# Kernel tuning notes

Measured on AMD Instinct MI355X. Metric: run time of the kernel, lower is better.

The kernel has to match this reference:

```python
import jax, jax.numpy as jnp
import numpy as np

NQ, NH = 7, 4          # quantiles x horizons
G = NQ * NH            # 28 independent branches
IN_DIM, H1, H2 = 64, 64, 32


def setup_inputs() -> dict:
    key = jax.random.key(0)
    ks = jax.random.split(key, 7)
    B = 131072
    x = jax.random.normal(ks[0], (B, IN_DIM), dtype=jnp.float32)
    s1 = 1.0 / np.sqrt(IN_DIM)
    s2 = 1.0 / np.sqrt(H1)
    s3 = 1.0 / np.sqrt(H2)
    W1 = jax.random.uniform(ks[1], (G, IN_DIM, H1), jnp.float32, -s1, s1)
    b1 = jax.random.uniform(ks[2], (G, H1), jnp.float32, -s1, s1)
    W2 = jax.random.uniform(ks[3], (G, H1, H2), jnp.float32, -s2, s2)
    b2 = jax.random.uniform(ks[4], (G, H2), jnp.float32, -s2, s2)
    W3 = jax.random.uniform(ks[5], (G, H2, 1), jnp.float32, -s3, s3)
    b3 = jax.random.uniform(ks[6], (G, 1), jnp.float32, -s3, s3)
    return {"x": x, "W1": W1, "b1": b1, "W2": W2, "b2": b2, "W3": W3, "b3": b3}


def reference(x, W1, b1, W2, b2, W3, b3):
    # All G branches fused as batched GEMMs. x: [B, in]
    B = x.shape[0]
    h = jax.nn.relu(jnp.einsum('bi,gij->gbj', x, W1) + b1[:, None, :])   # [G,B,H1]
    h = jax.nn.relu(jnp.einsum('gbj,gjk->gbk', h, W2) + b2[:, None, :])  # [G,B,H2]
    o = jnp.einsum('gbk,gko->gbo', h, W3) + b3[:, None, :]               # [G,B,1]
    # branch order matches nested loop: quantile outer, horizon inner
    out = o[..., 0].reshape(NQ, NH, B).transpose(2, 0, 1)                # [B,NQ,NH]
    return out
```

## Files before the change

kernel.cpp:

```cpp
#include <hip/hip_runtime.h>
#include <hip/hip_bf16.h>
#include <hip/hip_fp16.h>

#define GN 28
#define G_TILE_BYTES 12288
#define WS_BYTES (GN * G_TILE_BYTES)

typedef __attribute__((ext_vector_type(4))) float f32x4;
typedef __attribute__((ext_vector_type(8))) short short8;
typedef _Float16 f16x8 __attribute__((ext_vector_type(8)));
typedef __fp16 pk16x2 __attribute__((ext_vector_type(2)));

__device__ __forceinline__ unsigned short f2h(float v){
  __half h = __float2half(v);
  return __builtin_bit_cast(unsigned short, h);
}
__device__ __forceinline__ f32x4 mfma16f(short8 a, short8 b, f32x4 c){
  return __builtin_amdgcn_mfma_f32_16x16x32_f16(
      __builtin_bit_cast(f16x8, a), __builtin_bit_cast(f16x8, b), c, 0, 0, 0);
}

__global__ __launch_bounds__(256) void prep_weights(
    const float* __restrict__ W1, const float* __restrict__ W2,
    unsigned char* __restrict__ ws){
  __shared__ float t1[64*65];
  __shared__ float t2[64*33];
  const int g = blockIdx.x;
  const int tid = threadIdx.x;

  {
    const f32x4* src = (const f32x4*)(W1 + g*4096);
    int k = tid >> 2, n0 = (tid & 3) * 16;
    #pragma unroll
    for (int j = 0; j < 4; ++j){
      f32x4 v = src[tid*4 + j];
      #pragma unroll
      for (int e = 0; e < 4; ++e) t1[k*65 + n0 + j*4 + e] = v[e];
    }
  }
  {
    const f32x4* src = (const f32x4*)(W2 + g*2048);
    int k = tid >> 2, n0 = (tid & 3) * 8;
    #pragma unroll
    for (int j = 0; j < 2; ++j){
      f32x4 v = src[tid*2 + j];
      #pragma unroll
      for (int e = 0; e < 4; ++e) t2[k*33 + n0 + j*4 + e] = v[e];
    }
  }
  __syncthreads();

  unsigned char* base = ws + g*G_TILE_BYTES;
  {
    int n = tid & 63, mh = tid >> 6;
    #pragma unroll
    for (int h = 0; h < 2; ++h){
      unsigned w[4];
      #pragma unroll
      for (int mm = 0; mm < 4; ++mm){
        int m = mh*8 + h*4 + mm;
        float lo = t1[(2*m    )*65 + n];
        float hi = t1[(2*m + 1)*65 + n];
        w[mm] = (unsigned)f2h(lo) | ((unsigned)f2h(hi) << 16);
      }
      int off = (n*128 + mh*32 + h*16) ^ ((n & 7) << 4);
      *(uint4*)(base + off) = make_uint4(w[0], w[1], w[2], w[3]);
    }
  }
  {
    int n2 = tid & 31, mq = tid >> 5;
    unsigned w[4];
    #pragma unroll
    for (int mm = 0; mm < 4; ++mm){
      int m = mq*4 + mm;
      int kk = 2*m;
      int ks = kk >> 5, qq = (kk >> 3) & 3, u = (kk >> 2) & 1, i = kk & 3;
      int kn = 32*ks + 16*u + 4*qq + i;
      float lo = t2[(kn    )*33 + n2];
      float hi = t2[(kn + 1)*33 + n2];
      w[mm] = (unsigned)f2h(lo) | ((unsigned)f2h(hi) << 16);
    }
    int off = (n2*128 + mq*16) ^ ((n2 & 7) << 4);
    *(uint4*)(base + 8192 + off) = make_uint4(w[0], w[1], w[2], w[3]);
  }
}

__global__ __launch_bounds__(256, 4) void mlp_fused(
    const float* __restrict__ x,  const float* __restrict__ b1,
    const float* __restrict__ b2, const float* __restrict__ W3,
    const float* __restrict__ b3, const unsigned char* __restrict__ ws,
    float* __restrict__ out){
  __shared__ uint4 wbuf[2][768];
  __shared__ float outb[128*28];

  const int tid = threadIdx.x;
  const int wv  = tid >> 6;
  const int ln  = tid & 63;
  const int l15 = ln & 15;
  const int q   = ln >> 4;
  const int rowBase = blockIdx.x * 128 + wv * 32;

  short8 xf[2][2];
  #pragma unroll
  for (int rt = 0; rt < 2; ++rt)
    #pragma unroll
    for (int ks = 0; ks < 2; ++ks){
      const float* p = x + (rowBase + rt*16 + l15)*64 + ks*32 + q*8;
      f32x4 a = *(const f32x4*)p;
      f32x4 b = *(const f32x4*)(p + 4);
      short8 s;
      #pragma unroll
      for (int j = 0; j < 4; ++j){
        s[j]   = (short)f2h(a[j]);
        s[4+j] = (short)f2h(b[j]);
      }
      xf[rt][ks] = s;
    }

  int offA1[4][2], offA2[2][2];
  #pragma unroll
  for (int nt = 0; nt < 4; ++nt)
    #pragma unroll
    for (int ks = 0; ks < 2; ++ks){
      int n = nt*16 + l15;
      offA1[nt][ks] = ((n*128 + ks*64 + q*16) ^ ((n & 7) << 4)) >> 4;
    }
  #pragma unroll
  for (int nt = 0; nt < 2; ++nt)
    #pragma unroll
    for (int ks = 0; ks < 2; ++ks){
      int n2 = nt*16 + l15;
      offA2[nt][ks] = (((n2*128 + ks*64 + q*16) ^ ((n2 & 7) << 4)) >> 4) + 512;
    }

  auto stage = [&](int g, int buf){
    const unsigned char* gb = ws + g*G_TILE_BYTES + wv*3072 + ln*16;
    uint4* lb = &wbuf[buf][wv*192];
    #pragma unroll
    for (int it = 0; it < 3; ++it){
      __builtin_amdgcn_global_load_lds(
          (const __attribute__((address_space(1))) void*)(gb + it*1024),
          (__attribute__((address_space(3))) void*)(lb + it*64), 16, 0, 0);
    }
  };

  auto packrelu = [&](const f32x4& v0, const f32x4& v1) -> short8 {
    union { unsigned u[4]; short8 s; } r;
    pk16x2 t0 = __builtin_amdgcn_cvt_pkrtz(fmaxf(v0[0],0.f), fmaxf(v0[1],0.f));
    pk16x2 t1 = __builtin_amdgcn_cvt_pkrtz(fmaxf(v0[2],0.f), fmaxf(v0[3],0.f));
    pk16x2 t2 = __builtin_amdgcn_cvt_pkrtz(fmaxf(v1[0],0.f), fmaxf(v1[1],0.f));
    pk16x2 t3 = __builtin_amdgcn_cvt_pkrtz(fmaxf(v1[2],0.f), fmaxf(v1[3],0.f));
    r.u[0] = __builtin_bit_cast(unsigned, t0);
    r.u[1] = __builtin_bit_cast(unsigned, t1);
    r.u[2] = __builtin_bit_cast(unsigned, t2);
    r.u[3] = __builtin_bit_cast(unsigned, t3);
    return r.s;
  };

  auto body = [&](int g, f32x4 (&bC)[4], f32x4 (&bN)[4]){
    const int cur = g & 1;
    if (g + 1 < GN) stage(g + 1, cur ^ 1);

    const int gnext = (g + 1 < GN) ? g + 1 : GN - 1;
    #pragma unroll
    for (int nt = 0; nt < 4; ++nt)
      bN[nt] = *(const f32x4*)(b1 + gnext*64 + nt*16 + q*4);

    const uint4* wb = wbuf[cur];

    short8 a1[4][2];
    #pragma unroll
    for (int nt = 0; nt < 4; ++nt)
      #pragma unroll
      for (int ks = 0; ks < 2; ++ks)
        a1[nt][ks] = __builtin_bit_cast(short8, wb[offA1[nt][ks]]);
    f32x4 acc1[4][2];
    #pragma unroll
    for (int nt = 0; nt < 4; ++nt)
      #pragma unroll
      for (int rt = 0; rt < 2; ++rt){
        acc1[nt][rt] = mfma16f(a1[nt][0], xf[rt][0], bC[nt]);
        acc1[nt][rt] = mfma16f(a1[nt][1], xf[rt][1], acc1[nt][rt]);
      }

    f32x4 b2v[2], w3v[2];
    #pragma unroll
    for (int nt = 0; nt < 2; ++nt){
      b2v[nt] = *(const f32x4*)(b2 + g*32 + nt*16 + q*4);
      w3v[nt] = *(const f32x4*)(W3 + g*32 + nt*16 + q*4);
    }

    short8 bh[2][2];
    #pragma unroll
    for (int rt = 0; rt < 2; ++rt)
      #pragma unroll
      for (int ks = 0; ks < 2; ++ks)
        bh[rt][ks] = packrelu(acc1[2*ks][rt], acc1[2*ks + 1][rt]);

    short8 a2[2][2];
    #pragma unroll
    for (int nt = 0; nt < 2; ++nt)
      #pragma unroll
      for (int ks = 0; ks < 2; ++ks)
        a2[nt][ks] = __builtin_bit_cast(short8, wb[offA2[nt][ks]]);
    f32x4 acc2[2][2];
    #pragma unroll
    for (int nt = 0; nt < 2; ++nt)
      #pragma unroll
      for (int rt = 0; rt < 2; ++rt){
        acc2[nt][rt] = mfma16f(a2[nt][0], bh[rt][0], b2v[nt]);
        acc2[nt][rt] = mfma16f(a2[nt][1], bh[rt][1], acc2[nt][rt]);
      }

    float bias3 = b3[g];
    #pragma unroll
    for (int rt = 0; rt < 2; ++rt){
      float p = 0.0f;
      #pragma unroll
      for (int nt = 0; nt < 2; ++nt)
        #pragma unroll
        for (int i = 0; i < 4; ++i)
          p = fmaf(fmaxf(acc2[nt][rt][i], 0.0f), w3v[nt][i], p);
      p += __shfl_xor(p, 16);
      p += __shfl_xor(p, 32);
      p += bias3;
      if (ln < 16)
        outb[(wv*32 + rt*16 + ln)*28 + g] = p;
    }

    asm volatile("s_waitcnt vmcnt(0)" ::: "memory");
    __syncthreads();
  };

  f32x4 b1A[4], b1B[4];
  stage(0, 0);
  #pragma unroll
  for (int nt = 0; nt < 4; ++nt)
    b1A[nt] = *(const f32x4*)(b1 + 0*64 + nt*16 + q*4);
  asm volatile("s_waitcnt vmcnt(0)" ::: "memory");
  __syncthreads();

  for (int gg = 0; gg < GN; gg += 2){
    body(gg,     b1A, b1B);
    body(gg + 1, b1B, b1A);
  }

  const uint2* ob2 = (const uint2*)outb;
  uint2* og2 = (uint2*)(out + blockIdx.x * (128*28));
  #pragma unroll
  for (int i = 0; i < 7; ++i){
    int idx = i*256 + tid;
    og2[idx] = ob2[idx];
  }
}

extern "C" void kernel_launch(void* const* d_in, const int* in_sizes, int n_in,
                              void* d_out, int out_size, void* d_ws, size_t ws_size,
                              hipStream_t stream){
  const float* x  = (const float*)d_in[0];
  const float* W1 = (const float*)d_in[1];
  const float* b1 = (const float*)d_in[2];
  const float* W2 = (const float*)d_in[3];
  const float* b2 = (const float*)d_in[4];
  const float* W3 = (const float*)d_in[5];
  const float* b3 = (const float*)d_in[6];
  unsigned char* ws = (unsigned char*)d_ws;
  float* out = (float*)d_out;
  if (ws_size < (size_t)WS_BYTES) return;
  hipLaunchKernelGGL(prep_weights, dim3(GN), dim3(256), 0, stream, W1, W2, ws);
  hipLaunchKernelGGL(mlp_fused, dim3(1024), dim3(256), 0, stream,
                     x, b1, b2, W3, b3, ws, out);
}
```

Measured before the change: 144.3 us.

## Stage weights in chunks of three branches to cut barriers per block

Restructures the branch loop so each double-buffered LDS stage holds three branches' weights, which cuts the number of vmcnt waits and block barriers from 28 to 10. The output staging buffer is shrunk to a per-chunk double buffer, and each chunk's three columns are written straight to global memory with scalar strided stores. LDS use grows to roughly 76KB per block, so launch bounds drop to 2 blocks per CU, which lowers occupancy. The new output writes are narrow and uncoalesced.

```diff
diff --git a/kernel.cpp b/kernel.cpp
--- a/kernel.cpp
+++ b/kernel.cpp
@@ -3,6 +3,8 @@
 #include <hip/hip_fp16.h>
 
 #define GN 28
+#define CH 3
+#define NCH 10
 #define G_TILE_BYTES 12288
 #define WS_BYTES (GN * G_TILE_BYTES)
 
@@ -85,13 +87,13 @@
   }
 }
 
-__global__ __launch_bounds__(256, 4) void mlp_fused(
+__global__ __launch_bounds__(256, 2) void mlp_fused(
     const float* __restrict__ x,  const float* __restrict__ b1,
     const float* __restrict__ b2, const float* __restrict__ W3,
     const float* __restrict__ b3, const unsigned char* __restrict__ ws,
     float* __restrict__ out){
-  __shared__ uint4 wbuf[2][768];
-  __shared__ float outb[128*28];
+  __shared__ uint4 wbuf[2][CH*768];
+  __shared__ float outb[2][128*CH];
 
   const int tid = threadIdx.x;
   const int wv  = tid >> 6;
@@ -133,14 +135,20 @@
       offA2[nt][ks] = (((n2*128 + ks*64 + q*16) ^ ((n2 & 7) << 4)) >> 4) + 512;
     }
 
-  auto stage = [&](int g, int buf){
-    const unsigned char* gb = ws + g*G_TILE_BYTES + wv*3072 + ln*16;
-    uint4* lb = &wbuf[buf][wv*192];
-    #pragma unroll
-    for (int it = 0; it < 3; ++it){
-      __builtin_amdgcn_global_load_lds(
-          (const __attribute__((address_space(1))) void*)(gb + it*1024),
-          (__attribute__((address_space(3))) void*)(lb + it*64), 16, 0, 0);
+  auto stageChunk = [&](int ch, int buf){
+    #pragma unroll
+    for (int t = 0; t < CH; ++t){
+      int g = ch*CH + t;
+      if (g < GN){
+        const unsigned char* gb = ws + g*G_TILE_BYTES + wv*3072 + ln*16;
+        uint4* lb = &wbuf[buf][t*768 + wv*192];
+        #pragma unroll
+        for (int it = 0; it < 3; ++it){
+          __builtin_amdgcn_global_load_lds(
+              (const __attribute__((address_space(1))) void*)(gb + it*1024),
+              (__attribute__((address_space(3))) void*)(lb + it*64), 16, 0, 0);
+        }
+      }
     }
   };
 
@@ -157,100 +165,102 @@
     return r.s;
   };
 
-  auto body = [&](int g, f32x4 (&bC)[4], f32x4 (&bN)[4]){
-    const int cur = g & 1;
-    if (g + 1 < GN) stage(g + 1, cur ^ 1);
-
-    const int gnext = (g + 1 < GN) ? g + 1 : GN - 1;
-    #pragma unroll
-    for (int nt = 0; nt < 4; ++nt)
-      bN[nt] = *(const f32x4*)(b1 + gnext*64 + nt*16 + q*4);
-
+  stageChunk(0, 0);
+  asm volatile("s_waitcnt vmcnt(0)" ::: "memory");
+  __syncthreads();
+
+  for (int ch = 0; ch < NCH; ++ch){
+    const int cur = ch & 1;
+    if (ch + 1 < NCH) stageChunk(ch + 1, cur ^ 1);
     const uint4* wb = wbuf[cur];
-
-    short8 a1[4][2];
-    #pragma unroll
-    for (int nt = 0; nt < 4; ++nt)
-      #pragma unroll
-      for (int ks = 0; ks < 2; ++ks)
-        a1[nt][ks] = __builtin_bit_cast(short8, wb[offA1[nt][ks]]);
-    f32x4 acc1[4][2];
-    #pragma unroll
-    for (int nt = 0; nt < 4; ++nt)
+    float* ob = &outb[cur][0];
+
+    #pragma unroll
+    for (int t = 0; t < CH; ++t){
+      const int g = ch*CH + t;
+      if (g >= GN) continue;
+      const uint4* wt = wb + t*768;
+
+      f32x4 b1v[4];
+      #pragma unroll
+      for (int nt = 0; nt < 4; ++nt)
+        b1v[nt] = *(const f32x4*)(b1 + g*64 + nt*16 + q*4);
+
+      short8 a1[4][2];
+      #pragma unroll
+      for (int nt = 0; nt < 4; ++nt)
+        #pragma unroll
+        for (int ks = 0; ks < 2; ++ks)
+          a1[nt][ks] = __builtin_bit_cast(short8, wt[offA1[nt][ks]]);
+      f32x4 acc1[4][2];
+      #pragma unroll
+      for (int nt = 0; nt < 4; ++nt)
+        #pragma unroll
+        for (int rt = 0; rt < 2; ++rt){
+          acc1[nt][rt] = mfma16f(a1[nt][0], xf[rt][0], b1v[nt]);
+          acc1[nt][rt] = mfma16f(a1[nt][1], xf[rt][1], acc1[nt][rt]);
+        }
+
+      f32x4 b2v[2], w3v[2];
+      #pragma unroll
+      for (int nt = 0; nt < 2; ++nt){
+        b2v[nt] = *(const f32x4*)(b2 + g*32 + nt*16 + q*4);
+        w3v[nt] = *(const f32x4*)(W3 + g*32 + nt*16 + q*4);
+      }
+
+      short8 bh[2][2];
+      #pragma unroll
+      for (int rt = 0; rt < 2; ++rt)
+        #pragma unroll
+        for (int ks = 0; ks < 2; ++ks)
+          bh[rt][ks] = packrelu(acc1[2*ks][rt], acc1[2*ks + 1][rt]);
+
+      short8 a2[2][2];
+      #pragma unroll
+      for (int nt = 0; nt < 2; ++nt)
+        #pragma unroll
+        for (int ks = 0; ks < 2; ++ks)
+          a2[nt][ks] = __builtin_bit_cast(short8, wt[offA2[nt][ks]]);
+      f32x4 acc2[2][2];
+      #pragma unroll
+      for (int nt = 0; nt < 2; ++nt)
+        #pragma unroll
+        for (int rt = 0; rt < 2; ++rt){
+          acc2[nt][rt] = mfma16f(a2[nt][0], bh[rt][0], b2v[nt]);
+          acc2[nt][rt] = mfma16f(a2[nt][1], bh[rt][1], acc2[nt][rt]);
+        }
+
+      float bias3 = b3[g];
       #pragma unroll
       for (int rt = 0; rt < 2; ++rt){
-        acc1[nt][rt] = mfma16f(a1[nt][0], xf[rt][0], bC[nt]);
-        acc1[nt][rt] = mfma16f(a1[nt][1], xf[rt][1], acc1[nt][rt]);
-      }
-
-    f32x4 b2v[2], w3v[2];
-    #pragma unroll
-    for (int nt = 0; nt < 2; ++nt){
-      b2v[nt] = *(const f32x4*)(b2 + g*32 + nt*16 + q*4);
-      w3v[nt] = *(const f32x4*)(W3 + g*32 + nt*16 + q*4);
-    }
-
-    short8 bh[2][2];
-    #pragma unroll
-    for (int rt = 0; rt < 2; ++rt)
-      #pragma unroll
-      for (int ks = 0; ks < 2; ++ks)
-        bh[rt][ks] = packrelu(acc1[2*ks][rt], acc1[2*ks + 1][rt]);
-
-    short8 a2[2][2];
-    #pragma unroll
-    for (int nt = 0; nt < 2; ++nt)
-      #pragma unroll
-      for (int ks = 0; ks < 2; ++ks)
-        a2[nt][ks] = __builtin_bit_cast(short8, wb[offA2[nt][ks]]);
-    f32x4 acc2[2][2];
-    #pragma unroll
-    for (int nt = 0; nt < 2; ++nt)
-      #pragma unroll
-      for (int rt = 0; rt < 2; ++rt){
-        acc2[nt][rt] = mfma16f(a2[nt][0], bh[rt][0], b2v[nt]);
-        acc2[nt][rt] = mfma16f(a2[nt][1], bh[rt][1], acc2[nt][rt]);
-      }
-
-    float bias3 = b3[g];
-    #pragma unroll
-    for (int rt = 0; rt < 2; ++rt){
-      float p = 0.0f;
-      #pragma unroll
-      for (int nt = 0; nt < 2; ++nt)
-        #pragma unroll
-        for (int i = 0; i < 4; ++i)
-          p = fmaf(fmaxf(acc2[nt][rt][i], 0.0f), w3v[nt][i], p);
-      p += __shfl_xor(p, 16);
-      p += __shfl_xor(p, 32);
-      p += bias3;
-      if (ln < 16)
-        outb[(wv*32 + rt*16 + ln)*28 + g] = p;
+        float p = 0.0f;
+        #pragma unroll
+        for (int nt = 0; nt < 2; ++nt)
+          #pragma unroll
+          for (int i = 0; i < 4; ++i)
+            p = fmaf(fmaxf(acc2[nt][rt][i], 0.0f), w3v[nt][i], p);
+        p += __shfl_xor(p, 16);
+        p += __shfl_xor(p, 32);
+        p += bias3;
+        if (ln < 16)
+          ob[(wv*32 + rt*16 + ln)*CH + t] = p;
+      }
     }
 
     asm volatile("s_waitcnt vmcnt(0)" ::: "memory");
     __syncthreads();
-  };
-
-  f32x4 b1A[4], b1B[4];
-  stage(0, 0);
-  #pragma unroll
-  for (int nt = 0; nt < 4; ++nt)
-    b1A[nt] = *(const f32x4*)(b1 + 0*64 + nt*16 + q*4);
-  asm volatile("s_waitcnt vmcnt(0)" ::: "memory");
-  __syncthreads();
-
-  for (int gg = 0; gg < GN; gg += 2){
-    body(gg,     b1A, b1B);
-    body(gg + 1, b1B, b1A);
-  }
-
-  const uint2* ob2 = (const uint2*)outb;
-  uint2* og2 = (uint2*)(out + blockIdx.x * (128*28));
-  #pragma unroll
-  for (int i = 0; i < 7; ++i){
-    int idx = i*256 + tid;
-    og2[idx] = ob2[idx];
+
+    {
+      const int g0 = ch*CH;
+      const int nc = (GN - g0 < CH) ? (GN - g0) : CH;
+      if (tid < 128){
+        float* dst = out + (blockIdx.x*128 + tid)*GN + g0;
+        const float* src = &outb[cur][tid*CH];
+        #pragma unroll
+        for (int c = 0; c < CH; ++c)
+          if (c < nc) dst[c] = src[c];
+      }
+    }
   }
 }
 
```

After: 161.0 us. 1.12x slower.
